# Kernel tuning notes

Hardware: AMD Instinct MI355X
Metric: run time of the kernel (lower is better)

## Reference

```python
import jax, jax.numpy as jnp
import numpy as np

HEADS = 4


def setup_inputs() -> dict:
    key = jax.random.key(0)
    ks = jax.random.split(key, 6)
    b, c, d, h, w = 4, 512, 16, 16, 16
    x = jax.random.normal(ks[0], (b, c, d, h, w), dtype=jnp.float32)
    s = 0.02  # param init scale
    Wq = jax.random.normal(ks[1], (c, c), dtype=jnp.float32) * s
    Wk = jax.random.normal(ks[2], (c, c), dtype=jnp.float32) * s
    Wv = jax.random.normal(ks[3], (c, c), dtype=jnp.float32) * s
    Wproj = jax.random.normal(ks[4], (c, c), dtype=jnp.float32) * s
    bproj = jnp.zeros((c,), dtype=jnp.float32)
    return {"x": x, "Wq": Wq, "Wk": Wk, "Wv": Wv, "Wproj": Wproj, "bproj": bproj}


def reference(x, Wq, Wk, Wv, Wproj, bproj):
    b, c, d, h, w = x.shape
    N = d * h * w
    scale = (c // HEADS) ** -0.5  # module uses ch//heads for scale
    xf = x.reshape(b, c, N)  # (b, c, N)
    # 1x1 Conv1d == channel matmul
    q = jnp.einsum('oc,bcn->bon', Wq, xf)
    k = jnp.einsum('oc,bcn->bon', Wk, xf)
    v = jnp.einsum('oc,bcn->bon', Wv, xf)
    # Faithful to original (buggy) view: split SEQUENCE dim by heads -> (b, H, c, N//H)
    q = q.reshape(b, HEADS, c, N // HEADS)
    k = k.reshape(b, HEADS, c, N // HEADS)
    v = v.reshape(b, HEADS, c, N // HEADS)
    attn = jax.nn.softmax(jnp.einsum('bhqe,bhke->bhqk', q, k) * scale, axis=-1)
    out = jnp.einsum('bhqk,bhke->bhqe', attn, v)  # (b, H, c, N//H)
    out = jnp.swapaxes(out, 2, 3).reshape(b, c, N)  # matches transpose(2,3).view
    out = jnp.einsum('oc,bcn->bon', Wproj, out) + bproj[None, :, None]
    return out.reshape(b, c, d, h, w) + x
```

## Files before the change

kernel.cpp:

```cpp
#include <hip/hip_runtime.h>
#include <stdint.h>


typedef __attribute__((ext_vector_type(8))) short short8;
typedef __attribute__((ext_vector_type(4))) float f32x4;

typedef const __attribute__((address_space(1))) unsigned int* gas_ptr;
typedef __attribute__((address_space(3))) unsigned int* las_ptr;

#define ATTN_SCALE 0.08838834764831845f

__device__ __forceinline__ unsigned short f2bf(float f) {
    union { float f; unsigned int u; } c; c.f = f;
    unsigned int u = c.u;
    u += 0x7fffu + ((u >> 16) & 1u);
    return (unsigned short)(u >> 16);
}

__device__ __forceinline__ void gl_lds16(const void* g, void* l) {
    __builtin_amdgcn_global_load_lds((gas_ptr)(uintptr_t)g, (las_ptr)(uintptr_t)l,
                                     16, 0, 0);
}

template<int LDA, int LDB, int KDIM, bool PERMB = false>
__device__ __forceinline__ void mfma_core(
    const unsigned short* __restrict__ A,
    const unsigned short* __restrict__ B,
    int m0, int n0,
    unsigned short* __restrict__ sA, unsigned short* __restrict__ sB,
    f32x4 acc[4][4])
{
    const int tid  = threadIdx.x;
    const int lane = tid & 63, wave = tid >> 6;
    const int lr = lane >> 2, lc = lane & 3;
    const int lcs = lc ^ ((lr >> 1) & 3);
    const int wm = (wave & 1) * 64, wn = (wave >> 1) * 64;
    const int col = lane & 15, quad = lane >> 4;
    const int swz = (quad ^ ((col >> 1) & 3)) * 8;

    const unsigned short* ga = A + (size_t)(m0 + 32 * wave + lr) * LDA + lcs * 8;
    int rb0 = n0 + 32 * wave + lr;
    int rb1 = rb0 + 16;
    if (PERMB) {
        rb0 = 4 * (rb0 & 127) + (rb0 >> 7);
        rb1 = 4 * (rb1 & 127) + (rb1 >> 7);
    }
    const unsigned short* gb0 = B + (size_t)rb0 * LDB + lcs * 8;
    const unsigned short* gb1 = B + (size_t)rb1 * LDB + lcs * 8;

    const int wr0 = (32 * wave) * 32;
    const int wr1 = (32 * wave + 16) * 32;

    gl_lds16(ga,            sA + wr0);
    gl_lds16(ga + 16 * LDA, sA + wr1);
    gl_lds16(gb0,           sB + wr0);
    gl_lds16(gb1,           sB + wr1);

    constexpr int NK = KDIM / 32;
    for (int kk = 0; kk < NK; ++kk) {
        const int bo = (kk & 1) * 4096;
        if (kk + 1 < NK) {
            const int nb = ((kk + 1) & 1) * 4096;
            const int k0 = (kk + 1) * 32;
            gl_lds16(ga + k0,            sA + nb + wr0);
            gl_lds16(ga + k0 + 16 * LDA, sA + nb + wr1);
            gl_lds16(gb0 + k0,           sB + nb + wr0);
            gl_lds16(gb1 + k0,           sB + nb + wr1);
            asm volatile("s_waitcnt vmcnt(4)" ::: "memory");
        } else {
            asm volatile("s_waitcnt vmcnt(0)" ::: "memory");
        }
        __builtin_amdgcn_s_barrier();
        asm volatile("" ::: "memory");
        __builtin_amdgcn_sched_barrier(0);

        const unsigned short* bA = sA + bo;
        const unsigned short* bB = sB + bo;
        short8 af[4], bfv[4];
        #pragma unroll
        for (int i = 0; i < 4; ++i)
            af[i] = *(const short8*)&bA[(wm + i * 16 + col) * 32 + swz];
        #pragma unroll
        for (int j = 0; j < 4; ++j)
            bfv[j] = *(const short8*)&bB[(wn + j * 16 + col) * 32 + swz];
        #pragma unroll
        for (int i = 0; i < 4; ++i)
            #pragma unroll
            for (int j = 0; j < 4; ++j)
                acc[i][j] = __builtin_amdgcn_mfma_f32_16x16x32_bf16(
                    af[i], bfv[j], acc[i][j], 0, 0, 0);

        __builtin_amdgcn_s_barrier();
        asm volatile("" ::: "memory");
    }
}

__global__ __launch_bounds__(256)
void prep(const float* __restrict__ x,
          const float* __restrict__ Wq, const float* __restrict__ Wk,
          const float* __restrict__ Wv, const float* __restrict__ Wp,
          unsigned short* __restrict__ xT, unsigned short* __restrict__ Wb)
{
    if (blockIdx.z == 4) {
        const int idx = (blockIdx.y * 64 + blockIdx.x) * 256 + threadIdx.x;
        const int mat = idx >> 16;
        const int off = (idx & 65535) << 2;
        const float* src = (mat == 0 ? Wq : mat == 1 ? Wk : mat == 2 ? Wv : Wp) + off;
        const float4 f = *(const float4*)src;
        uint2 o;
        o.x = f2bf(f.x) | ((unsigned)f2bf(f.y) << 16);
        o.y = f2bf(f.z) | ((unsigned)f2bf(f.w) << 16);
        *(uint2*)&Wb[mat * 262144 + off] = o;
        return;
    }
    const int b = blockIdx.z;
    const int l = threadIdx.x & 63, w = threadIdx.x >> 6;
    const int n  = blockIdx.x * 64 + l;
    const int c0 = blockIdx.y * 32 + w * 8;
    const float* xp = x + (size_t)b * 2097152 + (size_t)c0 * 4096 + n;
    unsigned int p[4];
    #pragma unroll
    for (int j = 0; j < 4; ++j) {
        const unsigned short a  = f2bf(xp[(2 * j)     * 4096]);
        const unsigned short bb = f2bf(xp[(2 * j + 1) * 4096]);
        p[j] = a | ((unsigned)bb << 16);
    }
    uint4 v; v.x = p[0]; v.y = p[1]; v.z = p[2]; v.w = p[3];
    *(uint4*)&xT[(size_t)b * 2097152 + (size_t)n * 512 + c0] = v;
}

__global__ __launch_bounds__(256)
void gemm_qkv(const unsigned short* __restrict__ Wb,
              const unsigned short* __restrict__ xT,
              unsigned short* __restrict__ qb, unsigned short* __restrict__ kb,
              unsigned short* __restrict__ vT)
{
    __shared__ unsigned short sA[2 * 128 * 32], sB[2 * 128 * 32];

    const int z = blockIdx.z, wsel = z >> 2, b = z & 3;
    const unsigned short* A = Wb + wsel * 262144;
    const unsigned short* B = xT + (size_t)b * 2097152;
    const int m0 = blockIdx.y * 128, n0 = blockIdx.x * 128;

    f32x4 z4 = {0.f, 0.f, 0.f, 0.f};
    f32x4 acc[4][4];
    #pragma unroll
    for (int i = 0; i < 4; ++i)
        #pragma unroll
        for (int j = 0; j < 4; ++j) acc[i][j] = z4;

    mfma_core<512, 512, 512>(A, B, m0, n0, sA, sB, acc);

    const int lane = threadIdx.x & 63, wave = threadIdx.x >> 6;
    const int wm = (wave & 1) * 64, wn = (wave >> 1) * 64;
    const int col = lane & 15, quad = lane >> 4;

    if (wsel < 2) {
        unsigned short* C = (wsel == 0 ? qb : kb) + (size_t)b * 2097152;
        #pragma unroll
        for (int i = 0; i < 4; ++i)
            #pragma unroll
            for (int r = 0; r < 4; ++r) {
                const int row = m0 + wm + i * 16 + quad * 4 + r;
                #pragma unroll
                for (int j = 0; j < 4; ++j)
                    C[(size_t)row * 4096 + n0 + wn + j * 16 + col] = f2bf(acc[i][j][r]);
            }
    } else {
        const int h = m0 >> 7, s = n0 >> 10, e0 = n0 & 1023;
        unsigned short* dst = vT + (size_t)(b * 4 + h) * 524288 + s * 128;
        #pragma unroll
        for (int i = 0; i < 4; ++i) {
            const int kb2 = wm + i * 16 + quad * 4;
            #pragma unroll
            for (int j = 0; j < 4; ++j) {
                const int e = e0 + wn + j * 16 + col;
                uint2 o;
                o.x = f2bf(acc[i][j][0]) | ((unsigned)f2bf(acc[i][j][1]) << 16);
                o.y = f2bf(acc[i][j][2]) | ((unsigned)f2bf(acc[i][j][3]) << 16);
                *(uint2*)&dst[(size_t)e * 512 + kb2] = o;
            }
        }
    }
}

__global__ __launch_bounds__(256)
void gemm_qk(const unsigned short* __restrict__ qb,
             const unsigned short* __restrict__ kb,
             float* __restrict__ S)
{
    __shared__ unsigned short sA[2 * 128 * 32], sB[2 * 128 * 32];
    const int z = blockIdx.z;
    const int slab = z >> 1, half = z & 1;
    const unsigned short* A = qb + (size_t)slab * 524288 + half * 512;
    const unsigned short* B = kb + (size_t)slab * 524288 + half * 512;
    float* Sp = S + (size_t)half * 4194304 + (size_t)slab * 262144;
    const int m0 = blockIdx.y * 128, n0 = blockIdx.x * 128;

    f32x4 z4 = {0.f, 0.f, 0.f, 0.f};
    f32x4 acc[4][4];
    #pragma unroll
    for (int i = 0; i < 4; ++i)
        #pragma unroll
        for (int j = 0; j < 4; ++j) acc[i][j] = z4;

    mfma_core<1024, 1024, 512, true>(A, B, m0, n0, sA, sB, acc);

    const int lane = threadIdx.x & 63, wave = threadIdx.x >> 6;
    const int wm = (wave & 1) * 64, wn = (wave >> 1) * 64;
    const int col = lane & 15, quad = lane >> 4;
    #pragma unroll
    for (int i = 0; i < 4; ++i)
        #pragma unroll
        for (int r = 0; r < 4; ++r) {
            const int row = m0 + wm + i * 16 + quad * 4 + r;
            #pragma unroll
            for (int j = 0; j < 4; ++j)
                Sp[(size_t)row * 512 + n0 + wn + j * 16 + col] =
                    acc[i][j][r] * ATTN_SCALE;
        }
}

__global__ __launch_bounds__(256)
void softmax_rows(const float* __restrict__ S, unsigned short* __restrict__ P)
{
    const int wave = threadIdx.x >> 6, lane = threadIdx.x & 63;
    const int row  = blockIdx.x * 4 + wave;
    const float* p0 = S + (size_t)row * 512;
    const float* p1 = p0 + 4194304;
    unsigned short* o = P + (size_t)row * 512;

    float vals[8];
    float m = -1e30f;
    #pragma unroll
    for (int t = 0; t < 8; ++t) {
        vals[t] = p0[lane + t * 64] + p1[lane + t * 64];
        m = fmaxf(m, vals[t]);
    }
    #pragma unroll
    for (int s = 32; s > 0; s >>= 1) m = fmaxf(m, __shfl_xor(m, s));
    float sum = 0.f;
    #pragma unroll
    for (int t = 0; t < 8; ++t) { vals[t] = __expf(vals[t] - m); sum += vals[t]; }
    #pragma unroll
    for (int s = 32; s > 0; s >>= 1) sum += __shfl_xor(sum, s);
    const float inv = 1.f / sum;
    #pragma unroll
    for (int t = 0; t < 8; ++t) o[lane + t * 64] = f2bf(vals[t] * inv);
}

__global__ __launch_bounds__(256)
void gemm_pv(const unsigned short* __restrict__ Pb,
             const unsigned short* __restrict__ vT,
             unsigned short* __restrict__ yT)
{
    __shared__ unsigned short sT[128 * 136];
    unsigned short* sA = sT;
    unsigned short* sB = sT + 8192;
    const int z = blockIdx.z, b = z >> 2, hh = z & 3;
    const unsigned short* A = Pb + (size_t)z * 262144;
    const unsigned short* B = vT + (size_t)z * 524288;
    unsigned short* yTb = yT + (size_t)b * 2097152;
    const int m0 = blockIdx.y * 128;
    const int n0 = blockIdx.x * 128;

    f32x4 z4 = {0.f, 0.f, 0.f, 0.f};
    f32x4 acc[4][4];
    #pragma unroll
    for (int i = 0; i < 4; ++i)
        #pragma unroll
        for (int j = 0; j < 4; ++j) acc[i][j] = z4;

    mfma_core<512, 512, 512>(A, B, m0, n0, sA, sB, acc);

    __syncthreads();

    const int tid = threadIdx.x;
    const int lane = tid & 63, wave = tid >> 6;
    const int wm = (wave & 1) * 64, wn = (wave >> 1) * 64;
    const int col = lane & 15, quad = lane >> 4;

    #pragma unroll
    for (int i = 0; i < 4; ++i)
        #pragma unroll
        for (int r = 0; r < 4; ++r) {
            const int rr = wm + i * 16 + quad * 4 + r;
            #pragma unroll
            for (int j = 0; j < 4; ++j)
                sT[rr * 136 + wn + j * 16 + col] = f2bf(acc[i][j][r]);
        }
    __syncthreads();

    #pragma unroll
    for (int k = 0; k < 4; ++k) {
        const int rid = k * 256 + tid;
        const int qq_l = rid >> 3, s = rid & 7;
        const unsigned short* Trow = sT + qq_l * 136;
        unsigned int p[8];
        #pragma unroll
        for (int t = 0; t < 8; ++t) {
            const unsigned int a  = Trow[s + 8 * (2 * t)];
            const unsigned int bb = Trow[s + 8 * (2 * t + 1)];
            p[t] = a | (bb << 16);
        }
        const size_t base = (size_t)((s << 9) + m0 + qq_l) * 512 + hh * 128 + (n0 >> 3);
        uint4 lo; lo.x = p[0]; lo.y = p[1]; lo.z = p[2]; lo.w = p[3];
        uint4 hi; hi.x = p[4]; hi.y = p[5]; hi.z = p[6]; hi.w = p[7];
        *(uint4*)&yTb[base]     = lo;
        *(uint4*)&yTb[base + 8] = hi;
    }
}

__global__ __launch_bounds__(256)
void gemm_proj(const unsigned short* __restrict__ Wpb,
               const unsigned short* __restrict__ yT,
               const float* __restrict__ bias, const float* __restrict__ x,
               float* __restrict__ out)
{
    __shared__ unsigned short sA[2 * 128 * 32], sB[2 * 128 * 32];
    const int b = blockIdx.z;
    const unsigned short* B = yT + (size_t)b * 2097152;
    const int m0 = blockIdx.y * 128, n0 = blockIdx.x * 128;

    f32x4 z4 = {0.f, 0.f, 0.f, 0.f};
    f32x4 acc[4][4];
    #pragma unroll
    for (int i = 0; i < 4; ++i)
        #pragma unroll
        for (int j = 0; j < 4; ++j) acc[i][j] = z4;

    mfma_core<512, 512, 512>(Wpb, B, m0, n0, sA, sB, acc);

    const int lane = threadIdx.x & 63, wave = threadIdx.x >> 6;
    const int wm = (wave & 1) * 64, wn = (wave >> 1) * 64;
    const int col = lane & 15, quad = lane >> 4;
    const size_t boff = (size_t)b * 2097152;
    #pragma unroll
    for (int i = 0; i < 4; ++i)
        #pragma unroll
        for (int r = 0; r < 4; ++r) {
            const int row = m0 + wm + i * 16 + quad * 4 + r;
            const float bi = bias[row];
            #pragma unroll
            for (int j = 0; j < 4; ++j) {
                const size_t idx = boff + (size_t)row * 4096 + n0 + wn + j * 16 + col;
                out[idx] = acc[i][j][r] + bi + x[idx];
            }
        }
}

extern "C" void kernel_launch(void* const* d_in, const int* in_sizes, int n_in,
                              void* d_out, int out_size, void* d_ws, size_t ws_size,
                              hipStream_t stream) {
    const float* x     = (const float*)d_in[0];
    const float* Wq    = (const float*)d_in[1];
    const float* Wk    = (const float*)d_in[2];
    const float* Wv    = (const float*)d_in[3];
    const float* Wproj = (const float*)d_in[4];
    const float* bproj = (const float*)d_in[5];
    float* out = (float*)d_out;

    char* w = (char*)d_ws;
    unsigned short* xT = (unsigned short*)(w + 0);
    unsigned short* qb = (unsigned short*)(w + 16777216);
    unsigned short* kb = (unsigned short*)(w + 33554432);
    unsigned short* vT = (unsigned short*)(w + 50331648);
    float*          S  = (float*)        (w + 67108864);
    unsigned short* Pb = (unsigned short*)(w + 100663296);
    unsigned short* Wb = (unsigned short*)(w + 109051904);
    unsigned short* yT = xT;

    prep        <<<dim3(64, 16, 5),  256, 0, stream>>>(x, Wq, Wk, Wv, Wproj, xT, Wb);
    gemm_qkv    <<<dim3(32, 4, 12),  256, 0, stream>>>(Wb, xT, qb, kb, vT);
    gemm_qk     <<<dim3(4, 4, 32),   256, 0, stream>>>(qb, kb, S);
    softmax_rows<<<dim3(2048),       256, 0, stream>>>(S, Pb);
    gemm_pv     <<<dim3(8, 4, 16),   256, 0, stream>>>(Pb, vT, yT);
    gemm_proj   <<<dim3(32, 4, 4),   256, 0, stream>>>(Wb + 3 * 262144, yT, bproj, x, out);
}
```

Measured before the change: 199.0 us.

## Rewrite QKV GEMM with 256x256 tiles, 8 waves and ping-pong LDS pipeline

Replaces the 128x128, 4-wave QKV projection GEMM with a 256x256 tile kernel using 8 waves, direct global-to-LDS loads with XOR swizzling, and a split A/B staging schedule interleaved with MFMA phases under raised wave priority. Blocks are remapped through a flat-index permutation so neighbouring workgroups share operand tiles. The larger tile raises arithmetic intensity and the remap targets cache reuse. The cost is more accumulator registers per thread, fewer blocks (384), and hand-placed waitcnt and barrier logic that must stay exactly right.

```diff
diff --git a/kernel.cpp b/kernel.cpp
--- a/kernel.cpp
+++ b/kernel.cpp
@@ -129,55 +129,128 @@
     *(uint4*)&xT[(size_t)b * 2097152 + (size_t)n * 512 + c0] = v;
 }
 
-__global__ __launch_bounds__(256)
-void gemm_qkv(const unsigned short* __restrict__ Wb,
-              const unsigned short* __restrict__ xT,
-              unsigned short* __restrict__ qb, unsigned short* __restrict__ kb,
-              unsigned short* __restrict__ vT)
-{
-    __shared__ unsigned short sA[2 * 128 * 32], sB[2 * 128 * 32];
-
-    const int z = blockIdx.z, wsel = z >> 2, b = z & 3;
+__global__ __launch_bounds__(512, 2)
+void gemm_qkv8(const unsigned short* __restrict__ Wb,
+               const unsigned short* __restrict__ xT,
+               unsigned short* __restrict__ qb, unsigned short* __restrict__ kb,
+               unsigned short* __restrict__ vT)
+{
+    __shared__ unsigned short sA[2 * 256 * 32];
+    __shared__ unsigned short sB[2 * 256 * 32];
+
+    const int flat = blockIdx.x + 16 * blockIdx.y + 32 * blockIdx.z;
+    const int w2 = (flat & 7) * 48 + (flat >> 3);
+    const int nx = w2 & 15, ny = (w2 >> 4) & 1, nz = w2 >> 5;
+    const int wsel = nz >> 2, b = nz & 3;
     const unsigned short* A = Wb + wsel * 262144;
     const unsigned short* B = xT + (size_t)b * 2097152;
-    const int m0 = blockIdx.y * 128, n0 = blockIdx.x * 128;
+    const int m0 = ny * 256, n0 = nx * 256;
+
+    const int tid = threadIdx.x, lane = tid & 63, wave = tid >> 6;
+    const int wm8 = wave >> 2, wn8 = wave & 3;
+    const int col = lane & 15, quad = lane >> 4;
+    const int swz = (quad ^ ((col >> 1) & 3)) * 8;
+    const int r_loc = tid >> 2;
+    const int c4 = ((tid & 3) ^ ((r_loc >> 1) & 3)) * 8;
+
+    const unsigned short* gA0 = A + (size_t)(m0 + r_loc) * 512 + c4;
+    const unsigned short* gA1 = A + (size_t)(m0 + 128 + r_loc) * 512 + c4;
+    const unsigned short* gB0 = B + (size_t)(n0 + r_loc) * 512 + c4;
+    const unsigned short* gB1 = B + (size_t)(n0 + 128 + r_loc) * 512 + c4;
+    const int wdst = wave * 512;
+
+    auto stageA = [&](int kt) {
+        const int bo = (kt & 1) * 8192;
+        gl_lds16(gA0 + kt * 32, sA + bo + wdst);
+        gl_lds16(gA1 + kt * 32, sA + bo + 4096 + wdst);
+    };
+    auto stageB = [&](int kt) {
+        const int bo = (kt & 1) * 8192;
+        gl_lds16(gB0 + kt * 32, sB + bo + wdst);
+        gl_lds16(gB1 + kt * 32, sB + bo + 4096 + wdst);
+    };
 
     f32x4 z4 = {0.f, 0.f, 0.f, 0.f};
-    f32x4 acc[4][4];
-    #pragma unroll
-    for (int i = 0; i < 4; ++i)
+    f32x4 acc[8][4];
+    #pragma unroll
+    for (int i = 0; i < 8; ++i)
         #pragma unroll
         for (int j = 0; j < 4; ++j) acc[i][j] = z4;
 
-    mfma_core<512, 512, 512>(A, B, m0, n0, sA, sB, acc);
-
-    const int lane = threadIdx.x & 63, wave = threadIdx.x >> 6;
-    const int wm = (wave & 1) * 64, wn = (wave >> 1) * 64;
-    const int col = lane & 15, quad = lane >> 4;
+    short8 a[4], bfr[4];
+
+    stageA(0); stageB(0); stageB(1);
+    asm volatile("s_waitcnt vmcnt(2)" ::: "memory");
+    __builtin_amdgcn_s_barrier();
+    asm volatile("" ::: "memory");
+
+    for (int kt = 0; kt < 16; ++kt) {
+        const int bo = (kt & 1) * 8192;
+        #pragma unroll
+        for (int fi = 0; fi < 4; ++fi)
+            a[fi] = *(const short8*)&sA[bo + (wm8 * 128 + fi * 16 + col) * 32 + swz];
+        #pragma unroll
+        for (int g = 0; g < 4; ++g)
+            bfr[g] = *(const short8*)&sB[bo + (wn8 * 64 + g * 16 + col) * 32 + swz];
+        if (kt < 15) stageA(kt + 1);
+        __builtin_amdgcn_s_barrier();
+        asm volatile("s_waitcnt lgkmcnt(0)" ::: "memory");
+        __builtin_amdgcn_sched_barrier(0);
+        __builtin_amdgcn_s_setprio(1);
+        #pragma unroll
+        for (int fi = 0; fi < 4; ++fi)
+            #pragma unroll
+            for (int g = 0; g < 4; ++g)
+                acc[fi][g] = __builtin_amdgcn_mfma_f32_16x16x32_bf16(
+                    a[fi], bfr[g], acc[fi][g], 0, 0, 0);
+        __builtin_amdgcn_s_setprio(0);
+        __builtin_amdgcn_s_barrier();
+        asm volatile("" ::: "memory");
+        #pragma unroll
+        for (int fi = 0; fi < 4; ++fi)
+            a[fi] = *(const short8*)&sA[bo + (wm8 * 128 + 64 + fi * 16 + col) * 32 + swz];
+        if (kt < 14) stageB(kt + 2);
+        __builtin_amdgcn_s_barrier();
+        asm volatile("s_waitcnt lgkmcnt(0)" ::: "memory");
+        __builtin_amdgcn_sched_barrier(0);
+        __builtin_amdgcn_s_setprio(1);
+        #pragma unroll
+        for (int fi = 0; fi < 4; ++fi)
+            #pragma unroll
+            for (int g = 0; g < 4; ++g)
+                acc[4 + fi][g] = __builtin_amdgcn_mfma_f32_16x16x32_bf16(
+                    a[fi], bfr[g], acc[4 + fi][g], 0, 0, 0);
+        __builtin_amdgcn_s_setprio(0);
+        if (kt == 14) asm volatile("s_waitcnt vmcnt(0)" ::: "memory");
+        else          asm volatile("s_waitcnt vmcnt(2)" ::: "memory");
+        __builtin_amdgcn_s_barrier();
+        asm volatile("" ::: "memory");
+    }
 
     if (wsel < 2) {
         unsigned short* C = (wsel == 0 ? qb : kb) + (size_t)b * 2097152;
         #pragma unroll
-        for (int i = 0; i < 4; ++i)
+        for (int f = 0; f < 8; ++f)
             #pragma unroll
             for (int r = 0; r < 4; ++r) {
-                const int row = m0 + wm + i * 16 + quad * 4 + r;
+                const int row = m0 + wm8 * 128 + f * 16 + quad * 4 + r;
                 #pragma unroll
-                for (int j = 0; j < 4; ++j)
-                    C[(size_t)row * 4096 + n0 + wn + j * 16 + col] = f2bf(acc[i][j][r]);
+                for (int g = 0; g < 4; ++g)
+                    C[(size_t)row * 4096 + n0 + wn8 * 64 + g * 16 + col] =
+                        f2bf(acc[f][g][r]);
             }
     } else {
-        const int h = m0 >> 7, s = n0 >> 10, e0 = n0 & 1023;
+        const int h = (m0 >> 7) + wm8, s = n0 >> 10, e0 = n0 & 1023;
         unsigned short* dst = vT + (size_t)(b * 4 + h) * 524288 + s * 128;
         #pragma unroll
-        for (int i = 0; i < 4; ++i) {
-            const int kb2 = wm + i * 16 + quad * 4;
-            #pragma unroll
-            for (int j = 0; j < 4; ++j) {
-                const int e = e0 + wn + j * 16 + col;
+        for (int f = 0; f < 8; ++f) {
+            const int kb2 = f * 16 + quad * 4;
+            #pragma unroll
+            for (int g = 0; g < 4; ++g) {
+                const int e = e0 + wn8 * 64 + g * 16 + col;
                 uint2 o;
-                o.x = f2bf(acc[i][j][0]) | ((unsigned)f2bf(acc[i][j][1]) << 16);
-                o.y = f2bf(acc[i][j][2]) | ((unsigned)f2bf(acc[i][j][3]) << 16);
+                o.x = f2bf(acc[f][g][0]) | ((unsigned)f2bf(acc[f][g][1]) << 16);
+                o.y = f2bf(acc[f][g][2]) | ((unsigned)f2bf(acc[f][g][3]) << 16);
                 *(uint2*)&dst[(size_t)e * 512 + kb2] = o;
             }
         }
@@ -371,7 +444,7 @@
     unsigned short* yT = xT;
 
     prep        <<<dim3(64, 16, 5),  256, 0, stream>>>(x, Wq, Wk, Wv, Wproj, xT, Wb);
-    gemm_qkv    <<<dim3(32, 4, 12),  256, 0, stream>>>(Wb, xT, qb, kb, vT);
+    gemm_qkv8   <<<dim3(16, 2, 12),  512, 0, stream>>>(Wb, xT, qb, kb, vT);
     gemm_qk     <<<dim3(4, 4, 32),   256, 0, stream>>>(qb, kb, S);
     softmax_rows<<<dim3(2048),       256, 0, stream>>>(S, Pb);
     gemm_pv     <<<dim3(8, 4, 16),   256, 0, stream>>>(Pb, vT, yT);
```

Result: slower. 207.1 us (+4.1%).

## Fuse QK^T GEMM with row softmax, removing fp32 score round-trip

Applied to the files above, without the earlier changes.

Replaces the split-K QK GEMM plus separate softmax kernel with one kernel. Each block computes a full 32x512 score strip with MFMA, reading operands straight from global memory with no LDS staging, then does the row max and sum through shuffles and a small LDS reduction. It writes bf16 probabilities directly. This removes the fp32 S buffer write and re-read and one kernel launch. In exchange the grid is smaller (256 blocks), the split-K parallelism is gone, and the operand loads are uncoalesced and unshared.

```diff
diff --git a/kernel.cpp b/kernel.cpp
--- a/kernel.cpp
+++ b/kernel.cpp
@@ -185,68 +185,116 @@
 }
 
 __global__ __launch_bounds__(256)
-void gemm_qk(const unsigned short* __restrict__ qb,
-             const unsigned short* __restrict__ kb,
-             float* __restrict__ S)
-{
-    __shared__ unsigned short sA[2 * 128 * 32], sB[2 * 128 * 32];
-    const int z = blockIdx.z;
-    const int slab = z >> 1, half = z & 1;
-    const unsigned short* A = qb + (size_t)slab * 524288 + half * 512;
-    const unsigned short* B = kb + (size_t)slab * 524288 + half * 512;
-    float* Sp = S + (size_t)half * 4194304 + (size_t)slab * 262144;
-    const int m0 = blockIdx.y * 128, n0 = blockIdx.x * 128;
+void gemm_qks(const unsigned short* __restrict__ qb,
+              const unsigned short* __restrict__ kb,
+              unsigned short* __restrict__ P)
+{
+    __shared__ float red[2][32][4];
+    const int d = blockIdx.x + 16 * blockIdx.y;
+    const int flat = (d & 7) * 32 + (d >> 3);
+    const int rg = flat & 15, z = flat >> 4;
+    const unsigned short* Aq = qb + (size_t)z * 524288;
+    const unsigned short* Bk = kb + (size_t)z * 524288;
+    unsigned short* Pz = P + (size_t)z * 262144;
+
+    const int lane = threadIdx.x & 63, w = threadIdx.x >> 6;
+    const int col = lane & 15, quad = lane >> 4;
+
+    const unsigned short* a0 = Aq + (size_t)(rg * 32 + col) * 1024 + quad * 8;
+    const unsigned short* a1 = a0 + 16 * 1024;
+    const unsigned short* bp[8];
+    #pragma unroll
+    for (int g = 0; g < 8; ++g) {
+        const int n = w * 128 + g * 16 + col;
+        const int r = 4 * (n & 127) + (n >> 7);
+        bp[g] = Bk + (size_t)r * 1024 + quad * 8;
+    }
 
     f32x4 z4 = {0.f, 0.f, 0.f, 0.f};
-    f32x4 acc[4][4];
-    #pragma unroll
-    for (int i = 0; i < 4; ++i)
-        #pragma unroll
-        for (int j = 0; j < 4; ++j) acc[i][j] = z4;
-
-    mfma_core<1024, 1024, 512, true>(A, B, m0, n0, sA, sB, acc);
-
-    const int lane = threadIdx.x & 63, wave = threadIdx.x >> 6;
-    const int wm = (wave & 1) * 64, wn = (wave >> 1) * 64;
-    const int col = lane & 15, quad = lane >> 4;
-    #pragma unroll
-    for (int i = 0; i < 4; ++i)
+    f32x4 acc[2][8];
+    #pragma unroll
+    for (int f = 0; f < 2; ++f)
+        #pragma unroll
+        for (int g = 0; g < 8; ++g) acc[f][g] = z4;
+
+    #pragma unroll 2
+    for (int k0 = 0; k0 < 1024; k0 += 32) {
+        const short8 af0 = *(const short8*)(a0 + k0);
+        const short8 af1 = *(const short8*)(a1 + k0);
+        short8 bf[8];
+        #pragma unroll
+        for (int g = 0; g < 8; ++g) bf[g] = *(const short8*)(bp[g] + k0);
+        #pragma unroll
+        for (int g = 0; g < 8; ++g)
+            acc[0][g] = __builtin_amdgcn_mfma_f32_16x16x32_bf16(
+                af0, bf[g], acc[0][g], 0, 0, 0);
+        #pragma unroll
+        for (int g = 0; g < 8; ++g)
+            acc[1][g] = __builtin_amdgcn_mfma_f32_16x16x32_bf16(
+                af1, bf[g], acc[1][g], 0, 0, 0);
+    }
+
+    float mx[2][4];
+    #pragma unroll
+    for (int f = 0; f < 2; ++f)
         #pragma unroll
         for (int r = 0; r < 4; ++r) {
-            const int row = m0 + wm + i * 16 + quad * 4 + r;
-            #pragma unroll
-            for (int j = 0; j < 4; ++j)
-                Sp[(size_t)row * 512 + n0 + wn + j * 16 + col] =
-                    acc[i][j][r] * ATTN_SCALE;
-        }
-}
-
-__global__ __launch_bounds__(256)
-void softmax_rows(const float* __restrict__ S, unsigned short* __restrict__ P)
-{
-    const int wave = threadIdx.x >> 6, lane = threadIdx.x & 63;
-    const int row  = blockIdx.x * 4 + wave;
-    const float* p0 = S + (size_t)row * 512;
-    const float* p1 = p0 + 4194304;
-    unsigned short* o = P + (size_t)row * 512;
-
-    float vals[8];
-    float m = -1e30f;
-    #pragma unroll
-    for (int t = 0; t < 8; ++t) {
-        vals[t] = p0[lane + t * 64] + p1[lane + t * 64];
-        m = fmaxf(m, vals[t]);
-    }
-    #pragma unroll
-    for (int s = 32; s > 0; s >>= 1) m = fmaxf(m, __shfl_xor(m, s));
-    float sum = 0.f;
-    #pragma unroll
-    for (int t = 0; t < 8; ++t) { vals[t] = __expf(vals[t] - m); sum += vals[t]; }
-    #pragma unroll
-    for (int s = 32; s > 0; s >>= 1) sum += __shfl_xor(sum, s);
-    const float inv = 1.f / sum;
-    #pragma unroll
-    for (int t = 0; t < 8; ++t) o[lane + t * 64] = f2bf(vals[t] * inv);
+            float m = acc[f][0][r];
+            #pragma unroll
+            for (int g = 1; g < 8; ++g) m = fmaxf(m, acc[f][g][r]);
+            #pragma unroll
+            for (int s = 1; s < 16; s <<= 1) m = fmaxf(m, __shfl_xor(m, s));
+            mx[f][r] = m;
+        }
+    if (col == 0) {
+        #pragma unroll
+        for (int f = 0; f < 2; ++f)
+            #pragma unroll
+            for (int r = 0; r < 4; ++r)
+                red[0][f * 16 + quad * 4 + r][w] = mx[f][r];
+    }
+    __syncthreads();
+    float sm[2][4];
+    #pragma unroll
+    for (int f = 0; f < 2; ++f)
+        #pragma unroll
+        for (int r = 0; r < 4; ++r) {
+            const int row = f * 16 + quad * 4 + r;
+            const float m = fmaxf(fmaxf(red[0][row][0], red[0][row][1]),
+                                  fmaxf(red[0][row][2], red[0][row][3]));
+            float s = 0.f;
+            #pragma unroll
+            for (int g = 0; g < 8; ++g) {
+                const float e = __expf((acc[f][g][r] - m) * ATTN_SCALE);
+                acc[f][g][r] = e;
+                s += e;
+            }
+            #pragma unroll
+            for (int t = 1; t < 16; t <<= 1) s += __shfl_xor(s, t);
+            sm[f][r] = s;
+        }
+    if (col == 0) {
+        #pragma unroll
+        for (int f = 0; f < 2; ++f)
+            #pragma unroll
+            for (int r = 0; r < 4; ++r)
+                red[1][f * 16 + quad * 4 + r][w] = sm[f][r];
+    }
+    __syncthreads();
+    #pragma unroll
+    for (int f = 0; f < 2; ++f)
+        #pragma unroll
+        for (int r = 0; r < 4; ++r) {
+            const int row = f * 16 + quad * 4 + r;
+            const float tot = red[1][row][0] + red[1][row][1]
+                            + red[1][row][2] + red[1][row][3];
+            const float inv = 1.f / tot;
+            unsigned short* op = Pz + (size_t)(rg * 32 + row) * 512
+                               + w * 128 + col;
+            #pragma unroll
+            for (int g = 0; g < 8; ++g)
+                op[g * 16] = f2bf(acc[f][g][r] * inv);
+        }
 }
 
 __global__ __launch_bounds__(256)
@@ -365,15 +413,13 @@
     unsigned short* qb = (unsigned short*)(w + 16777216);
     unsigned short* kb = (unsigned short*)(w + 33554432);
     unsigned short* vT = (unsigned short*)(w + 50331648);
-    float*          S  = (float*)        (w + 67108864);
     unsigned short* Pb = (unsigned short*)(w + 100663296);
     unsigned short* Wb = (unsigned short*)(w + 109051904);
     unsigned short* yT = xT;
 
     prep        <<<dim3(64, 16, 5),  256, 0, stream>>>(x, Wq, Wk, Wv, Wproj, xT, Wb);
     gemm_qkv    <<<dim3(32, 4, 12),  256, 0, stream>>>(Wb, xT, qb, kb, vT);
-    gemm_qk     <<<dim3(4, 4, 32),   256, 0, stream>>>(qb, kb, S);
-    softmax_rows<<<dim3(2048),       256, 0, stream>>>(S, Pb);
+    gemm_qks    <<<dim3(16, 16),     256, 0, stream>>>(qb, kb, Pb);
     gemm_pv     <<<dim3(8, 4, 16),   256, 0, stream>>>(Pb, vT, yT);
     gemm_proj   <<<dim3(32, 4, 4),   256, 0, stream>>>(Wb + 3 * 262144, yT, bproj, x, out);
 }
```

Result: slower. 215.8 us (+8.5%).
